# Optimization experiments

Measured on AMD Instinct MI355X. Metric: run time of the kernel, lower is better.

Reference implementation:

```python
import jax, jax.numpy as jnp
import numpy as np

N = 8192
E = 262144


def gcn_layer(x, w, row, col, edge_weight, n_nodes):
    # support = x @ W ; out = A_sparse @ support (COO spmm via segment_sum)
    support = x @ w                              # [N, d_out]
    msg = support[col] * edge_weight[:, None]    # gather + scale, [E, d_out]
    return jax.ops.segment_sum(msg, row, num_segments=n_nodes)  # [N, d_out]


def setup_inputs() -> dict:
    key = jax.random.key(0)
    k1, k2, k3, k4, k5, k6 = jax.random.split(key, 6)
    x = jax.random.normal(k1, (N, 512), dtype=jnp.float32)
    w1 = jax.random.normal(k2, (512, 256), dtype=jnp.float32) * 0.05
    w2 = jax.random.normal(k3, (256, 16), dtype=jnp.float32) * 0.05
    edge_weight = jax.random.uniform(k4, (E,), dtype=jnp.float32)
    row = jax.random.randint(k5, (E,), 0, N, dtype=jnp.int32)
    col = jax.random.randint(k6, (E,), 0, N, dtype=jnp.int32)
    return {"x": x, "w1": w1, "w2": w2, "edge_weight": edge_weight,
            "row": row, "col": col}


def reference(x, w1, w2, edge_weight, row, col):
    # gc1: dropout(identity at eval) -> linear -> spmm -> relu
    h1 = jax.nn.relu(gcn_layer(x, w1, row, col, edge_weight, N))
    # gc2: identity activation
    z = gcn_layer(h1, w2, row, col, edge_weight, N)          # [N, 16]
    # InnerProductDecoder with act = identity (dropout off at eval)
    adj = z @ z.T                                            # [N, N]
    return adj
```

## Files before the change

kernel.cpp:

```cpp
#include <hip/hip_runtime.h>

#define NN 8192
#define NE 262144
#define DIN 512
#define DH 256
#define DZ 16

typedef __attribute__((ext_vector_type(8))) short bf16x8;
typedef __attribute__((ext_vector_type(4))) float f32x4;

__device__ __forceinline__ ushort f2bf(float f) {
    uint u = __float_as_uint(f);
    uint r = (u + 0x7FFFu + ((u >> 16) & 1u)) >> 16;
    return (ushort)r;
}
__device__ __forceinline__ float bf2f(ushort h) {
    return __uint_as_float((uint)h << 16);
}

__global__ void k_prep_hist(const float* __restrict__ W, ushort* __restrict__ WBf,
                            const int* __restrict__ row, int* __restrict__ cnt) {
    int b = blockIdx.x;
    int t = threadIdx.x;
    if (b < 512) {
        int o = b * 256 + t;
        int n = o >> 9, k = o & 511;
        WBf[o] = f2bf(W[(size_t)k * DH + n]);
    } else {
        int e = (b - 512) * 256 + t;
        atomicAdd(&cnt[row[e]], 1);
    }
}

__global__ __launch_bounds__(1024) void k_scan(const int* __restrict__ cnt,
                                               int* __restrict__ row_ptr,
                                               int* __restrict__ cursor) {
    __shared__ int wsum[16];
    int t = threadIdx.x;
    int wave = t >> 6, lane = t & 63;
    int4 v0 = *(const int4*)&cnt[t * 8];
    int4 v1 = *(const int4*)&cnt[t * 8 + 4];
    int local[8] = {v0.x, v0.y, v0.z, v0.w, v1.x, v1.y, v1.z, v1.w};
    int s = 0;
#pragma unroll
    for (int j = 0; j < 8; j++) s += local[j];
    int si = s;
#pragma unroll
    for (int off = 1; off < 64; off <<= 1) {
        int u = __shfl_up(si, off);
        if (lane >= off) si += u;
    }
    if (lane == 63) wsum[wave] = si;
    __syncthreads();
    if (t < 16) {
        int w = wsum[t];
#pragma unroll
        for (int off = 1; off < 16; off <<= 1) {
            int u = __shfl_up(w, off);
            if (t >= off) w += u;
        }
        wsum[t] = w;
    }
    __syncthreads();
    int base = (wave ? wsum[wave - 1] : 0) + si - s;
#pragma unroll
    for (int j = 0; j < 8; j++) {
        row_ptr[t * 8 + j] = base;
        cursor[t * 8 + j]  = base;
        base += local[j];
    }
    if (t == 1023) row_ptr[NN] = base;
}

__global__ void k_scatter(const int* __restrict__ row, const int* __restrict__ col,
                          const float* __restrict__ ew, int* __restrict__ cursor,
                          int* __restrict__ col_s, float* __restrict__ w_s) {
    int e = blockIdx.x * blockDim.x + threadIdx.x;
    if (e < NE) {
        int r = row[e];
        int pos = atomicAdd(&cursor[r], 1);
        col_s[pos] = col[e];
        w_s[pos]   = ew[e];
    }
}

__global__ __launch_bounds__(256) void k_gemm1_mfma(const float* __restrict__ X,
                                                    const ushort* __restrict__ B,
                                                    ushort* __restrict__ O) {
    __shared__ ushort As[32][72];
    __shared__ ushort Bs[256][72];
    int t = threadIdx.x;
    int wave = t >> 6, lane = t & 63;
    int m0 = blockIdx.x * 32;
    int fr = lane & 15, fg = lane >> 4;
    int ar = t >> 3, ac = (t & 7) * 8;
    f32x4 acc[2][4] = {};
    for (int k0 = 0; k0 < DIN; k0 += 64) {
        __syncthreads();
        {
            const float* xp = &X[(size_t)(m0 + ar) * DIN + k0 + ac];
            float4 f0 = *(const float4*)&xp[0];
            float4 f1 = *(const float4*)&xp[4];
            ushort u[8] = {f2bf(f0.x), f2bf(f0.y), f2bf(f0.z), f2bf(f0.w),
                           f2bf(f1.x), f2bf(f1.y), f2bf(f1.z), f2bf(f1.w)};
            *(bf16x8*)&As[ar][ac] = *(const bf16x8*)&u[0];
        }
#pragma unroll
        for (int uix = 0; uix < 8; ++uix) {
            int u = uix * 256 + t;
            int brow = u >> 3, bcol = (u & 7) * 8;
            *(bf16x8*)&Bs[brow][bcol] = *(const bf16x8*)&B[(size_t)brow * DIN + k0 + bcol];
        }
        __syncthreads();
#pragma unroll
        for (int kk = 0; kk < 2; ++kk) {
            bf16x8 af[2], bb[4];
#pragma unroll
            for (int i = 0; i < 2; ++i)
                af[i] = *(const bf16x8*)&As[i * 16 + fr][kk * 32 + fg * 8];
#pragma unroll
            for (int j = 0; j < 4; ++j)
                bb[j] = *(const bf16x8*)&Bs[wave * 64 + j * 16 + fr][kk * 32 + fg * 8];
#pragma unroll
            for (int i = 0; i < 2; ++i)
#pragma unroll
                for (int j = 0; j < 4; ++j)
                    acc[i][j] = __builtin_amdgcn_mfma_f32_16x16x32_bf16(
                        af[i], bb[j], acc[i][j], 0, 0, 0);
        }
    }
#pragma unroll
    for (int i = 0; i < 2; ++i)
#pragma unroll
        for (int j = 0; j < 4; ++j)
#pragma unroll
            for (int r = 0; r < 4; ++r)
                O[(size_t)(m0 + i * 16 + fg * 4 + r) * DH + wave * 64 + j * 16 + fr] =
                    f2bf(acc[i][j][r]);
}

__global__ __launch_bounds__(256) void k_spmm1_gemm2(const ushort* __restrict__ Sbf,
                                                     const int* __restrict__ rp,
                                                     const int* __restrict__ cs,
                                                     const float* __restrict__ wsrt,
                                                     const float* __restrict__ W2,
                                                     float* __restrict__ S2) {
    __shared__ float w2s[DH * DZ];
    __shared__ float hs[2][DH];
    int t = threadIdx.x;
#pragma unroll
    for (int i = t; i < DH * DZ / 4; i += 256)
        ((float4*)w2s)[i] = ((const float4*)W2)[i];
    int sub = t >> 7;
    int ht = t & 127;
    int r = blockIdx.x * 2 + sub;
    int e0 = rp[r], e1 = rp[r + 1];
    float a0 = 0.f, a1 = 0.f, b0 = 0.f, b1 = 0.f;
    float c0 = 0.f, c1 = 0.f, d0 = 0.f, d1 = 0.f;
    int e = e0;
    for (; e + 3 < e1; e += 4) {
        int k0 = cs[e], k1 = cs[e + 1], k2 = cs[e + 2], k3 = cs[e + 3];
        float w0 = wsrt[e], w1 = wsrt[e + 1], w2_ = wsrt[e + 2], w3 = wsrt[e + 3];
        uint p0 = *(const uint*)&Sbf[(size_t)k0 * DH + ht * 2];
        uint p1 = *(const uint*)&Sbf[(size_t)k1 * DH + ht * 2];
        uint p2 = *(const uint*)&Sbf[(size_t)k2 * DH + ht * 2];
        uint p3 = *(const uint*)&Sbf[(size_t)k3 * DH + ht * 2];
        a0 += w0 * bf2f((ushort)p0); a1 += w0 * bf2f((ushort)(p0 >> 16));
        b0 += w1 * bf2f((ushort)p1); b1 += w1 * bf2f((ushort)(p1 >> 16));
        c0 += w2_ * bf2f((ushort)p2); c1 += w2_ * bf2f((ushort)(p2 >> 16));
        d0 += w3 * bf2f((ushort)p3); d1 += w3 * bf2f((ushort)(p3 >> 16));
    }
    for (; e < e1; ++e) {
        float w0 = wsrt[e];
        uint p0 = *(const uint*)&Sbf[(size_t)cs[e] * DH + ht * 2];
        a0 += w0 * bf2f((ushort)p0); a1 += w0 * bf2f((ushort)(p0 >> 16));
    }
    float2 o;
    o.x = fmaxf(a0 + b0 + c0 + d0, 0.f);
    o.y = fmaxf(a1 + b1 + c1 + d1, 0.f);
    *(float2*)&hs[sub][ht * 2] = o;
    __syncthreads();
    int j = (t >> 3) & 15, g = t & 7;
    float acc = 0.f;
#pragma unroll
    for (int kk = 0; kk < 32; ++kk) {
        int k = g * 32 + kk;
        acc += hs[sub][k] * w2s[k * DZ + j];
    }
    acc += __shfl_xor(acc, 1);
    acc += __shfl_xor(acc, 2);
    acc += __shfl_xor(acc, 4);
    if (g == 0) S2[(size_t)r * DZ + j] = acc;
}

__global__ __launch_bounds__(256) void k_spmm2(const float* __restrict__ S2,
                                               const int* __restrict__ rp,
                                               const int* __restrict__ cs,
                                               const float* __restrict__ wsrt,
                                               ushort* __restrict__ ZHi,
                                               ushort* __restrict__ ZLo) {
    int t = threadIdx.x;
    int rl = t >> 4, c = t & 15;
    int r = blockIdx.x * 16 + rl;
    int e0 = rp[r], e1 = rp[r + 1];
    float acc = 0.f;
    for (int e = e0; e < e1; ++e) acc += wsrt[e] * S2[(size_t)cs[e] * DZ + c];
    ushort h = f2bf(acc);
    ZHi[(size_t)r * DZ + c] = h;
    ZLo[(size_t)r * DZ + c] = f2bf(acc - bf2f(h));
}

__global__ __launch_bounds__(256) void k_gemm3_mfma(const ushort* __restrict__ ZHi,
                                                    const ushort* __restrict__ ZLo,
                                                    float* __restrict__ O) {
    int t = threadIdx.x;
    int wave = t >> 6, lane = t & 63;
    int rb = blockIdx.y * 128 + (wave >> 1) * 64;
    int cb = blockIdx.x * 128 + (wave & 1) * 64;
    int fr = lane & 15, fg = lane >> 4;
    int ko = (fg & 1) * 8;
    const ushort* asel = (fg < 2) ? ZHi : ZLo;

    bf16x8 cpack[4], rhi[4], rlo[4];
    bf16x8 zero8 = {};
#pragma unroll
    for (int j = 0; j < 4; ++j)
        cpack[j] = *(const bf16x8*)&asel[(size_t)(cb + j * 16 + fr) * DZ + ko];
#pragma unroll
    for (int i = 0; i < 4; ++i) {
        rhi[i] = *(const bf16x8*)&ZHi[(size_t)(rb + i * 16 + fr) * DZ + ko];
        rlo[i] = (fg < 2) ? *(const bf16x8*)&ZLo[(size_t)(rb + i * 16 + fr) * DZ + ko]
                          : zero8;
    }
    f32x4 acc[4][4] = {};
#pragma unroll
    for (int i = 0; i < 4; ++i)
#pragma unroll
        for (int j = 0; j < 4; ++j) {
            acc[i][j] = __builtin_amdgcn_mfma_f32_16x16x32_bf16(cpack[j], rhi[i],
                                                                acc[i][j], 0, 0, 0);
            acc[i][j] = __builtin_amdgcn_mfma_f32_16x16x32_bf16(cpack[j], rlo[i],
                                                                acc[i][j], 0, 0, 0);
        }
#pragma unroll
    for (int i = 0; i < 4; ++i)
#pragma unroll
        for (int j = 0; j < 4; ++j)
            *(f32x4*)&O[(size_t)(rb + i * 16 + fr) * NN + cb + j * 16 + fg * 4] = acc[i][j];
}

extern "C" void kernel_launch(void* const* d_in, const int* in_sizes, int n_in,
                              void* d_out, int out_size, void* d_ws, size_t ws_size,
                              hipStream_t stream) {
    const float* x  = (const float*)d_in[0];
    const float* w1 = (const float*)d_in[1];
    const float* w2 = (const float*)d_in[2];
    const float* ew = (const float*)d_in[3];
    const int*  row = (const int*)d_in[4];
    const int*  col = (const int*)d_in[5];
    float* out = (float*)d_out;

    char* ws = (char*)d_ws;
    int*    row_ptr = (int*)ws;
    int*    cursor  = (int*)(ws + 36864);
    ushort* zhi     = (ushort*)(ws + 73728);
    ushort* zlo     = (ushort*)(ws + 73728 + 262144);

    char* ob = (char*)d_out;
    ushort* support1 = (ushort*)ob;
    float*  s2       = (float*)(ob + 16u * 1024 * 1024);
    int*    col_s    = (int*)(ob + 17u * 1024 * 1024);
    float*  w_s      = (float*)(ob + 18u * 1024 * 1024);
    ushort* w1tbf    = (ushort*)(ob + 36u * 1024 * 1024);

    hipMemsetAsync(cursor, 0, NN * sizeof(int), stream);
    k_prep_hist<<<1536, 256, 0, stream>>>(w1, w1tbf, row, cursor);
    k_scan<<<1, 1024, 0, stream>>>(cursor, row_ptr, cursor);
    k_scatter<<<NE / 256, 256, 0, stream>>>(row, col, ew, cursor, col_s, w_s);

    k_gemm1_mfma<<<NN / 32, 256, 0, stream>>>(x, w1tbf, support1);
    k_spmm1_gemm2<<<NN / 2, 256, 0, stream>>>(support1, row_ptr, col_s, w_s, w2, s2);

    k_spmm2<<<NN / 16, 256, 0, stream>>>(s2, row_ptr, col_s, w_s, zhi, zlo);

    k_gemm3_mfma<<<dim3(NN / 128, NN / 128), 256, 0, stream>>>(zhi, zlo, out);
}
```

Measured before the change: 148.3 us.

## Fuse edge scatter into GEMM1 kernel and stage edge lists in LDS for SpMM1

```diff
diff --git a/kernel.cpp b/kernel.cpp
--- a/kernel.cpp
+++ b/kernel.cpp
@@ -72,24 +72,26 @@
     if (t == 1023) row_ptr[NN] = base;
 }
 
-__global__ void k_scatter(const int* __restrict__ row, const int* __restrict__ col,
-                          const float* __restrict__ ew, int* __restrict__ cursor,
-                          int* __restrict__ col_s, float* __restrict__ w_s) {
-    int e = blockIdx.x * blockDim.x + threadIdx.x;
-    if (e < NE) {
-        int r = row[e];
-        int pos = atomicAdd(&cursor[r], 1);
-        col_s[pos] = col[e];
-        w_s[pos]   = ew[e];
-    }
-}
-
-__global__ __launch_bounds__(256) void k_gemm1_mfma(const float* __restrict__ X,
-                                                    const ushort* __restrict__ B,
-                                                    ushort* __restrict__ O) {
+__global__ __launch_bounds__(256) void k_gemm1_scatter(
+    const float* __restrict__ X, const ushort* __restrict__ B,
+    ushort* __restrict__ O,
+    const int* __restrict__ ROW, const int* __restrict__ COL,
+    const float* __restrict__ EW, int* __restrict__ cursor,
+    int* __restrict__ col_s, float* __restrict__ w_s) {
     __shared__ ushort As[32][72];
     __shared__ ushort Bs[256][72];
     int t = threadIdx.x;
+    {
+        int gid0 = blockIdx.x * 256 + t;
+#pragma unroll
+        for (int it = 0; it < 4; ++it) {
+            int e = gid0 + it * 65536;
+            int r = ROW[e];
+            int pos = atomicAdd(&cursor[r], 1);
+            col_s[pos] = COL[e];
+            w_s[pos]   = EW[e];
+        }
+    }
     int wave = t >> 6, lane = t & 63;
     int m0 = blockIdx.x * 32;
     int fr = lane & 15, fg = lane >> 4;
@@ -147,6 +149,8 @@
                                                      float* __restrict__ S2) {
     __shared__ float w2s[DH * DZ];
     __shared__ float hs[2][DH];
+    __shared__ int   ecs[2][64];
+    __shared__ float ews[2][64];
     int t = threadIdx.x;
 #pragma unroll
     for (int i = t; i < DH * DZ / 4; i += 256)
@@ -157,27 +161,37 @@
     int e0 = rp[r], e1 = rp[r + 1];
     float a0 = 0.f, a1 = 0.f, b0 = 0.f, b1 = 0.f;
     float c0 = 0.f, c1 = 0.f, d0 = 0.f, d1 = 0.f;
-    int e = e0;
-    for (; e + 3 < e1; e += 4) {
-        int k0 = cs[e], k1 = cs[e + 1], k2 = cs[e + 2], k3 = cs[e + 3];
-        float w0 = wsrt[e], w1 = wsrt[e + 1], w2_ = wsrt[e + 2], w3 = wsrt[e + 3];
-        uint p0 = *(const uint*)&Sbf[(size_t)k0 * DH + ht * 2];
-        uint p1 = *(const uint*)&Sbf[(size_t)k1 * DH + ht * 2];
-        uint p2 = *(const uint*)&Sbf[(size_t)k2 * DH + ht * 2];
-        uint p3 = *(const uint*)&Sbf[(size_t)k3 * DH + ht * 2];
-        a0 += w0 * bf2f((ushort)p0); a1 += w0 * bf2f((ushort)(p0 >> 16));
-        b0 += w1 * bf2f((ushort)p1); b1 += w1 * bf2f((ushort)(p1 >> 16));
-        c0 += w2_ * bf2f((ushort)p2); c1 += w2_ * bf2f((ushort)(p2 >> 16));
-        d0 += w3 * bf2f((ushort)p3); d1 += w3 * bf2f((ushort)(p3 >> 16));
-    }
-    for (; e < e1; ++e) {
-        float w0 = wsrt[e];
-        uint p0 = *(const uint*)&Sbf[(size_t)cs[e] * DH + ht * 2];
-        a0 += w0 * bf2f((ushort)p0); a1 += w0 * bf2f((ushort)(p0 >> 16));
+    for (int base = e0; base < e1; base += 64) {
+        int nv = min(64, e1 - base);
+        __syncthreads();
+        if (ht < 64 && ht < nv) {
+            ecs[sub][ht] = cs[base + ht];
+            ews[sub][ht] = wsrt[base + ht];
+        }
+        __syncthreads();
+        int e = 0;
+        for (; e + 3 < nv; e += 4) {
+            int k0 = ecs[sub][e], k1 = ecs[sub][e + 1], k2 = ecs[sub][e + 2], k3 = ecs[sub][e + 3];
+            float w0 = ews[sub][e], w1 = ews[sub][e + 1], w2_ = ews[sub][e + 2], w3 = ews[sub][e + 3];
+            uint p0 = *(const uint*)&Sbf[(size_t)k0 * DH + ht * 2];
+            uint p1 = *(const uint*)&Sbf[(size_t)k1 * DH + ht * 2];
+            uint p2 = *(const uint*)&Sbf[(size_t)k2 * DH + ht * 2];
+            uint p3 = *(const uint*)&Sbf[(size_t)k3 * DH + ht * 2];
+            a0 += w0 * bf2f((ushort)p0); a1 += w0 * bf2f((ushort)(p0 >> 16));
+            b0 += w1 * bf2f((ushort)p1); b1 += w1 * bf2f((ushort)(p1 >> 16));
+            c0 += w2_ * bf2f((ushort)p2); c1 += w2_ * bf2f((ushort)(p2 >> 16));
+            d0 += w3 * bf2f((ushort)p3); d1 += w3 * bf2f((ushort)(p3 >> 16));
+        }
+        for (; e < nv; ++e) {
+            float w0 = ews[sub][e];
+            uint p0 = *(const uint*)&Sbf[(size_t)ecs[sub][e] * DH + ht * 2];
+            a0 += w0 * bf2f((ushort)p0); a1 += w0 * bf2f((ushort)(p0 >> 16));
+        }
     }
     float2 o;
     o.x = fmaxf(a0 + b0 + c0 + d0, 0.f);
     o.y = fmaxf(a1 + b1 + c1 + d1, 0.f);
+    __syncthreads();
     *(float2*)&hs[sub][ht * 2] = o;
     __syncthreads();
     int j = (t >> 3) & 15, g = t & 7;
@@ -276,9 +290,9 @@
     hipMemsetAsync(cursor, 0, NN * sizeof(int), stream);
     k_prep_hist<<<1536, 256, 0, stream>>>(w1, w1tbf, row, cursor);
     k_scan<<<1, 1024, 0, stream>>>(cursor, row_ptr, cursor);
-    k_scatter<<<NE / 256, 256, 0, stream>>>(row, col, ew, cursor, col_s, w_s);
-
-    k_gemm1_mfma<<<NN / 32, 256, 0, stream>>>(x, w1tbf, support1);
+
+    k_gemm1_scatter<<<NN / 32, 256, 0, stream>>>(x, w1tbf, support1,
+                                                 row, col, ew, cursor, col_s, w_s);
     k_spmm1_gemm2<<<NN / 2, 256, 0, stream>>>(support1, row_ptr, col_s, w_s, w2, s2);
 
     k_spmm2<<<NN / 16, 256, 0, stream>>>(s2, row_ptr, col_s, w_s, zhi, zlo);
```

Result: faster. 140.3 us (-5.4%).
